# Performance work log

Measured on AMD Instinct MI355X. Metric: run time of the kernel, lower is better.

The kernel has to match this reference:

```python
import jax, jax.numpy as jnp
import numpy as np

N_ENT = 100000   # n_entities
N_REL = 40       # n_relations_ckg
D = 64           # embed_dim
L = 3            # n_layers
E = 1000000      # number of CKG triples (edges)


def setup_inputs() -> dict:
    key = jax.random.key(0)
    k = jax.random.split(key, 6)
    xavier = np.sqrt(6.0 / (D + D))  # xavier_uniform for square Linear
    return {
        "heads": jax.random.randint(k[0], (E,), 0, N_ENT),
        "rels": jax.random.randint(k[1], (E,), 0, N_REL),
        "tails": jax.random.randint(k[2], (E,), 0, N_ENT),
        "entity_embed": 0.01 * jax.random.normal(k[3], (N_ENT, D), dtype=jnp.float32),
        "rel_embeds": 0.01 * jax.random.normal(k[4], (L, N_REL, D), dtype=jnp.float32),
        "Ws": (jax.random.uniform(k[5], (L, D, D), minval=-1.0, maxval=1.0) * xavier).astype(jnp.float32),
    }


def _kgat_layer(h, heads, rels, tails, rel_emb, W):
    # h: [N, D]; heads/rels/tails: [E]; rel_emb: [n_rel, D]; W: [D, D] (nn.Linear weight)
    n = h.shape[0]
    e_h = h[heads]            # [E, D] gather
    e_t = h[tails]            # [E, D] gather
    e_r = rel_emb[rels]       # [E, D] gather
    # pi(h,r,t) = e_t . tanh(e_h + e_r)
    score = jnp.sum(e_t * jnp.tanh(e_h + e_r), axis=-1)          # [E]
    score = score - jax.lax.stop_gradient(jnp.max(score))        # global shift (detach)
    score_exp = jnp.exp(score)                                   # [E]
    score_sum = jax.ops.segment_sum(score_exp, heads, num_segments=n)  # [N]
    attn = score_exp / (score_sum[heads] + 1e-10)                # [E] per-head softmax
    agg = jax.ops.segment_sum(attn[:, None] * e_t, heads, num_segments=n)  # [N, D]
    out = (h + agg) @ W.T                                        # Linear, no bias
    return jax.nn.leaky_relu(out, negative_slope=0.2)            # dropout = identity (eval)


def reference(heads, rels, tails, entity_embed, rel_embeds, Ws):
    h = entity_embed
    all_layers = [h]
    for l in range(rel_embeds.shape[0]):
        h = _kgat_layer(h, heads, rels, tails, rel_embeds[l], Ws[l])
        all_layers.append(h)
    return jnp.concatenate(all_layers, axis=-1)  # [N, D*(L+1)]
```

## Files before the change

### kernel.cpp

```cpp
#include <hip/hip_runtime.h>

#define DD 64
#define ROW 256
#define CHUNK 1024

__global__ void k_copy_embed(const float* __restrict__ ent, float* __restrict__ out, int n_rows) {
    int idx = blockIdx.x * blockDim.x + threadIdx.x;
    int total = n_rows * 16;
    if (idx >= total) return;
    int n = idx >> 4, q = idx & 15;
    const float4* src = (const float4*)(ent + (long)n * DD);
    float4* dst = (float4*)(out + (long)n * ROW);
    dst[q] = src[q];
}

__global__ void k_count(const int* __restrict__ heads, int* __restrict__ counts, int nE) {
    int e = blockIdx.x * 256 + threadIdx.x;
    if (e >= nE) return;
    atomicAdd(counts + heads[e], 1);
}

__global__ __launch_bounds__(256) void k_scan_chunk(
        const int* __restrict__ counts, int* __restrict__ offs,
        int* __restrict__ partials, int n) {
    __shared__ int lds[256];
    int base = blockIdx.x * CHUNK;
    int t = threadIdx.x;
    int c[4]; int sum = 0;
    #pragma unroll
    for (int j = 0; j < 4; ++j) {
        int i = base + t * 4 + j;
        c[j] = (i < n) ? counts[i] : 0;
        sum += c[j];
    }
    lds[t] = sum; __syncthreads();
    for (int d = 1; d < 256; d <<= 1) {
        int v = (t >= d) ? lds[t - d] : 0;
        __syncthreads();
        lds[t] += v;
        __syncthreads();
    }
    int excl = lds[t] - sum;
    if (t == 255) partials[blockIdx.x] = lds[255];
    int run = excl;
    #pragma unroll
    for (int j = 0; j < 4; ++j) {
        int i = base + t * 4 + j;
        if (i < n) offs[i] = run;
        run += c[j];
    }
}

__global__ __launch_bounds__(128) void k_scan_part(int* __restrict__ partials, int nb) {
    __shared__ int lds[128];
    int t = threadIdx.x;
    int v = (t < nb) ? partials[t] : 0;
    lds[t] = v; __syncthreads();
    for (int d = 1; d < 128; d <<= 1) {
        int u = (t >= d) ? lds[t - d] : 0;
        __syncthreads();
        lds[t] += u;
        __syncthreads();
    }
    if (t < nb) partials[t] = lds[t] - v;
}

__global__ void k_scan_add(int* __restrict__ offs, int* __restrict__ running,
                           const int* __restrict__ partials, int n, int nE) {
    int i = blockIdx.x * 256 + threadIdx.x;
    if (i < n) {
        int v = offs[i] + partials[i >> 10];
        offs[i] = v;
        running[i] = v;
    } else if (i == n) {
        offs[n] = nE;
    }
}

__global__ void k_scatter(const int* __restrict__ heads, const int* __restrict__ rels,
                          const int* __restrict__ tails, int* __restrict__ running,
                          int* __restrict__ packed, int nE) {
    int e = blockIdx.x * 256 + threadIdx.x;
    if (e >= nE) return;
    int h = heads[e];
    int pos = atomicAdd(running + h, 1);
    packed[pos] = tails[e] | (rels[e] << 20);
}

__global__ __launch_bounds__(256) void k_layer(
        const int* __restrict__ offs, const int* __restrict__ packed,
        const float* __restrict__ hbase, const float* __restrict__ relemb,
        const float* __restrict__ W, float* __restrict__ outbase,
        int n_heads, int nE) {
    __shared__ float Wt[DD * 65];
    __shared__ float xs[4][DD];
    for (int idx = threadIdx.x; idx < DD * DD; idx += 256)
        Wt[(idx & 63) * 65 + (idx >> 6)] = W[idx];
    __syncthreads();

    int w = threadIdx.x >> 6, lane = threadIdx.x & 63;
    int g = lane >> 4, s = lane & 15;

    for (int hd = blockIdx.x * 4 + w; hd < n_heads; hd += gridDim.x * 4) {
        const float4 eh4 = *(const float4*)(hbase + (long)hd * ROW + 4 * s);
        float4 acc = make_float4(0.f, 0.f, 0.f, 0.f);
        float ssum = 0.f;
        int p0 = offs[hd], pe = offs[hd + 1];

        for (int cbase = p0; cbase < pe; cbase += 64) {
            int clen = min(pe - cbase, 64);
            int vAll = packed[min(cbase + lane, nE - 1)];

            int i0 = (g < clen) ? g : 0;
            int i1 = (4 + g < clen) ? 4 + g : 0;
            int v0 = __shfl(vAll, i0);
            int v1 = __shfl(vAll, i1);
            float4 tt0 = *(const float4*)(hbase + (long)(v0 & 0xFFFFF) * ROW + 4 * s);
            float4 rr0 = *(const float4*)(relemb + (v0 >> 20) * DD + 4 * s);
            float4 tt1 = *(const float4*)(hbase + (long)(v1 & 0xFFFFF) * ROW + 4 * s);
            float4 rr1 = *(const float4*)(relemb + (v1 >> 20) * DD + 4 * s);

            for (int i = 0; i < clen; i += 8) {
                int ia = i + 8 + g;  ia = (ia < clen) ? ia : 0;
                int ib = i + 12 + g; ib = (ib < clen) ? ib : 0;
                int va = __shfl(vAll, ia);
                int vb = __shfl(vAll, ib);
                float4 tta = *(const float4*)(hbase + (long)(va & 0xFFFFF) * ROW + 4 * s);
                float4 rra = *(const float4*)(relemb + (va >> 20) * DD + 4 * s);
                float4 ttb = *(const float4*)(hbase + (long)(vb & 0xFFFFF) * ROW + 4 * s);
                float4 rrb = *(const float4*)(relemb + (vb >> 20) * DD + 4 * s);

                {
                    float sc = 0.f;
                    #pragma unroll
                    for (int q = 0; q < 4; ++q) {
                        float xq = (&eh4.x)[q] + (&rr0.x)[q];
                        float t = __expf(2.f * xq);
                        float th = 1.f - 2.f * __builtin_amdgcn_rcpf(t + 1.f);
                        sc += (&tt0.x)[q] * th;
                    }
                    #pragma unroll
                    for (int off = 1; off <= 8; off <<= 1) sc += __shfl_xor(sc, off);
                    float se = ((i + g) < clen) ? __expf(sc) : 0.f;
                    ssum += se;
                    acc.x += se * tt0.x; acc.y += se * tt0.y;
                    acc.z += se * tt0.z; acc.w += se * tt0.w;
                }
                {
                    float sc = 0.f;
                    #pragma unroll
                    for (int q = 0; q < 4; ++q) {
                        float xq = (&eh4.x)[q] + (&rr1.x)[q];
                        float t = __expf(2.f * xq);
                        float th = 1.f - 2.f * __builtin_amdgcn_rcpf(t + 1.f);
                        sc += (&tt1.x)[q] * th;
                    }
                    #pragma unroll
                    for (int off = 1; off <= 8; off <<= 1) sc += __shfl_xor(sc, off);
                    float se = ((i + 4 + g) < clen) ? __expf(sc) : 0.f;
                    ssum += se;
                    acc.x += se * tt1.x; acc.y += se * tt1.y;
                    acc.z += se * tt1.z; acc.w += se * tt1.w;
                }
                tt0 = tta; rr0 = rra; tt1 = ttb; rr1 = rrb;
            }
        }

        #pragma unroll
        for (int off = 16; off <= 32; off <<= 1) {
            acc.x += __shfl_xor(acc.x, off);
            acc.y += __shfl_xor(acc.y, off);
            acc.z += __shfl_xor(acc.z, off);
            acc.w += __shfl_xor(acc.w, off);
            ssum  += __shfl_xor(ssum,  off);
        }
        float inv = 1.f / (ssum + 1e-10f);
        float4 x4;
        x4.x = eh4.x + acc.x * inv;  x4.y = eh4.y + acc.y * inv;
        x4.z = eh4.z + acc.z * inv;  x4.w = eh4.w + acc.w * inv;
        if (g == 0) *(float4*)(&xs[w][4 * s]) = x4;

        float y = 0.f;
        const float* xw = xs[w];
        #pragma unroll
        for (int k4 = 0; k4 < DD; k4 += 4) {
            float4 xv = *(const float4*)(xw + k4);
            y += xv.x * Wt[(k4 + 0) * 65 + lane];
            y += xv.y * Wt[(k4 + 1) * 65 + lane];
            y += xv.z * Wt[(k4 + 2) * 65 + lane];
            y += xv.w * Wt[(k4 + 3) * 65 + lane];
        }
        y = y >= 0.f ? y : 0.2f * y;
        outbase[(long)hd * ROW + lane] = y;
    }
}

extern "C" void kernel_launch(void* const* d_in, const int* in_sizes, int n_in,
                              void* d_out, int out_size, void* d_ws, size_t ws_size,
                              hipStream_t stream) {
    const int*   heads = (const int*)d_in[0];
    const int*   rels  = (const int*)d_in[1];
    const int*   tails = (const int*)d_in[2];
    const float* ent   = (const float*)d_in[3];
    const float* rel   = (const float*)d_in[4];
    const float* Ws    = (const float*)d_in[5];
    float* out = (float*)d_out;

    const int nE = in_sizes[0];
    const int N  = in_sizes[3] / DD;
    const int L  = in_sizes[5] / (DD * DD);
    const int NREL = in_sizes[4] / (L * DD);

    int* offs    = (int*)d_ws;
    int* running = offs + (N + 1);
    int* packed  = running + N;
    int* partials = packed + nE - 128;

    dim3 blk(256);
    int copy_blocks = (N * 16 + 255) / 256;
    int nchunks = (N + CHUNK - 1) / CHUNK;

    k_copy_embed<<<copy_blocks, blk, 0, stream>>>(ent, out, N);

    hipMemsetAsync(running, 0, (size_t)N * sizeof(int), stream);
    k_count<<<(nE + 255) / 256, blk, 0, stream>>>(heads, running, nE);
    k_scan_chunk<<<nchunks, blk, 0, stream>>>(running, offs, partials, N);
    k_scan_part<<<1, 128, 0, stream>>>(partials, nchunks);
    k_scan_add<<<(N + 1 + 255) / 256, blk, 0, stream>>>(offs, running, partials, N, nE);
    k_scatter<<<(nE + 255) / 256, blk, 0, stream>>>(heads, rels, tails, running, packed, nE);

    for (int l = 0; l < L; ++l) {
        k_layer<<<2048, blk, 0, stream>>>(
            offs, packed, out + l * DD, rel + (long)l * NREL * DD,
            Ws + (long)l * DD * DD, out + (l + 1) * DD, N, nE);
    }
}
```

Baseline: 503.4 us.

## Use polynomial tanh fast path, single-edge pipeline, and two-head batched matvec

Replaces the exp/rcp tanh with an odd minimax polynomial for small arguments, falling back to the exact form when any lane's argument exceeds a threshold. Given the small embedding values, the fallback should rarely fire. The edge loop now handles one edge group per iteration with a rolling prefetch depth of two. Each warp also processes two heads before a shared-memory matvec that reads W as float4 rows, which amortizes weight loads. The costs are an extra wave-wide vote per edge and shallower unrolling of the gather loop.

```diff
diff --git a/kernel.cpp b/kernel.cpp
--- a/kernel.cpp
+++ b/kernel.cpp
@@ -92,106 +92,111 @@
         const float* __restrict__ hbase, const float* __restrict__ relemb,
         const float* __restrict__ W, float* __restrict__ outbase,
         int n_heads, int nE) {
-    __shared__ float Wt[DD * 65];
-    __shared__ float xs[4][DD];
+    __shared__ float Wr[DD * 68];
+    __shared__ float xs[4][2][DD];
     for (int idx = threadIdx.x; idx < DD * DD; idx += 256)
-        Wt[(idx & 63) * 65 + (idx >> 6)] = W[idx];
+        Wr[(idx >> 6) * 68 + (idx & 63)] = W[idx];
     __syncthreads();
 
     int w = threadIdx.x >> 6, lane = threadIdx.x & 63;
     int g = lane >> 4, s = lane & 15;
-
-    for (int hd = blockIdx.x * 4 + w; hd < n_heads; hd += gridDim.x * 4) {
-        const float4 eh4 = *(const float4*)(hbase + (long)hd * ROW + 4 * s);
-        float4 acc = make_float4(0.f, 0.f, 0.f, 0.f);
-        float ssum = 0.f;
-        int p0 = offs[hd], pe = offs[hd + 1];
-
-        for (int cbase = p0; cbase < pe; cbase += 64) {
-            int clen = min(pe - cbase, 64);
-            int vAll = packed[min(cbase + lane, nE - 1)];
-
-            int i0 = (g < clen) ? g : 0;
-            int i1 = (4 + g < clen) ? 4 + g : 0;
-            int v0 = __shfl(vAll, i0);
-            int v1 = __shfl(vAll, i1);
-            float4 tt0 = *(const float4*)(hbase + (long)(v0 & 0xFFFFF) * ROW + 4 * s);
-            float4 rr0 = *(const float4*)(relemb + (v0 >> 20) * DD + 4 * s);
-            float4 tt1 = *(const float4*)(hbase + (long)(v1 & 0xFFFFF) * ROW + 4 * s);
-            float4 rr1 = *(const float4*)(relemb + (v1 >> 20) * DD + 4 * s);
-
-            for (int i = 0; i < clen; i += 8) {
-                int ia = i + 8 + g;  ia = (ia < clen) ? ia : 0;
-                int ib = i + 12 + g; ib = (ib < clen) ? ib : 0;
-                int va = __shfl(vAll, ia);
-                int vb = __shfl(vAll, ib);
-                float4 tta = *(const float4*)(hbase + (long)(va & 0xFFFFF) * ROW + 4 * s);
-                float4 rra = *(const float4*)(relemb + (va >> 20) * DD + 4 * s);
-                float4 ttb = *(const float4*)(hbase + (long)(vb & 0xFFFFF) * ROW + 4 * s);
-                float4 rrb = *(const float4*)(relemb + (vb >> 20) * DD + 4 * s);
-
-                {
-                    float sc = 0.f;
+    int wg = blockIdx.x * 4 + w;
+    int stride = gridDim.x * 4 * 2;
+
+    for (int hd0 = wg * 2; hd0 < n_heads; hd0 += stride) {
+        int nh = min(2, n_heads - hd0);
+
+        for (int hi = 0; hi < nh; ++hi) {
+            int hd = hd0 + hi;
+            const float4 eh4 = *(const float4*)(hbase + (long)hd * ROW + 4 * s);
+            float4 acc = make_float4(0.f, 0.f, 0.f, 0.f);
+            float ssum = 0.f;
+            int p0 = offs[hd], pe = offs[hd + 1];
+
+            for (int cbase = p0; cbase < pe; cbase += 64) {
+                int clen = min(pe - cbase, 64);
+                int vAll = packed[min(cbase + lane, nE - 1)];
+
+                int i0 = (g < clen) ? g : 0;
+                int i1 = (4 + g < clen) ? 4 + g : 0;
+                int v0 = __shfl(vAll, i0);
+                int v1 = __shfl(vAll, i1);
+                float4 tt0 = *(const float4*)(hbase + (long)(v0 & 0xFFFFF) * ROW + 4 * s);
+                float4 rr0 = *(const float4*)(relemb + (v0 >> 20) * DD + 4 * s);
+                float4 tt1 = *(const float4*)(hbase + (long)(v1 & 0xFFFFF) * ROW + 4 * s);
+                float4 rr1 = *(const float4*)(relemb + (v1 >> 20) * DD + 4 * s);
+
+                for (int i = 0; i < clen; i += 4) {
+                    int ipf = i + 8 + g; ipf = (ipf < clen) ? ipf : 0;
+                    int vp = __shfl(vAll, ipf);
+                    float4 ttp = *(const float4*)(hbase + (long)(vp & 0xFFFFF) * ROW + 4 * s);
+                    float4 rrp = *(const float4*)(relemb + (vp >> 20) * DD + 4 * s);
+
+                    float sc = 0.f, ax = 0.f;
                     #pragma unroll
                     for (int q = 0; q < 4; ++q) {
-                        float xq = (&eh4.x)[q] + (&rr0.x)[q];
-                        float t = __expf(2.f * xq);
-                        float th = 1.f - 2.f * __builtin_amdgcn_rcpf(t + 1.f);
-                        sc += (&tt0.x)[q] * th;
+                        float x = (&eh4.x)[q] + (&rr0.x)[q];
+                        float z = x * x;
+                        float p = fmaf(z, -5.70498872745e-3f, 2.06390887954e-2f);
+                        p = fmaf(z, p, -5.37397155531e-2f);
+                        p = fmaf(z, p, 1.33314422036e-1f);
+                        p = fmaf(z, p, -3.33332819422e-1f);
+                        float th = fmaf(x * z, p, x);
+                        ax = fmaxf(ax, fabsf(x));
+                        sc = fmaf((&tt0.x)[q], th, sc);
+                    }
+                    if (__any(ax > 0.625f)) {
+                        sc = 0.f;
+                        #pragma unroll
+                        for (int q = 0; q < 4; ++q) {
+                            float x = (&eh4.x)[q] + (&rr0.x)[q];
+                            float t = __expf(2.f * x);
+                            float th = 1.f - 2.f * __builtin_amdgcn_rcpf(t + 1.f);
+                            sc = fmaf((&tt0.x)[q], th, sc);
+                        }
                     }
                     #pragma unroll
                     for (int off = 1; off <= 8; off <<= 1) sc += __shfl_xor(sc, off);
                     float se = ((i + g) < clen) ? __expf(sc) : 0.f;
                     ssum += se;
-                    acc.x += se * tt0.x; acc.y += se * tt0.y;
-                    acc.z += se * tt0.z; acc.w += se * tt0.w;
+                    acc.x = fmaf(se, tt0.x, acc.x);
+                    acc.y = fmaf(se, tt0.y, acc.y);
+                    acc.z = fmaf(se, tt0.z, acc.z);
+                    acc.w = fmaf(se, tt0.w, acc.w);
+
+                    tt0 = tt1; rr0 = rr1; tt1 = ttp; rr1 = rrp;
                 }
-                {
-                    float sc = 0.f;
-                    #pragma unroll
-                    for (int q = 0; q < 4; ++q) {
-                        float xq = (&eh4.x)[q] + (&rr1.x)[q];
-                        float t = __expf(2.f * xq);
-                        float th = 1.f - 2.f * __builtin_amdgcn_rcpf(t + 1.f);
-                        sc += (&tt1.x)[q] * th;
-                    }
-                    #pragma unroll
-                    for (int off = 1; off <= 8; off <<= 1) sc += __shfl_xor(sc, off);
-                    float se = ((i + 4 + g) < clen) ? __expf(sc) : 0.f;
-                    ssum += se;
-                    acc.x += se * tt1.x; acc.y += se * tt1.y;
-                    acc.z += se * tt1.z; acc.w += se * tt1.w;
-                }
-                tt0 = tta; rr0 = rra; tt1 = ttb; rr1 = rrb;
             }
+
+            #pragma unroll
+            for (int off = 16; off <= 32; off <<= 1) {
+                acc.x += __shfl_xor(acc.x, off);
+                acc.y += __shfl_xor(acc.y, off);
+                acc.z += __shfl_xor(acc.z, off);
+                acc.w += __shfl_xor(acc.w, off);
+                ssum  += __shfl_xor(ssum,  off);
+            }
+            float inv = 1.f / (ssum + 1e-10f);
+            float4 x4;
+            x4.x = eh4.x + acc.x * inv;  x4.y = eh4.y + acc.y * inv;
+            x4.z = eh4.z + acc.z * inv;  x4.w = eh4.w + acc.w * inv;
+            if (g == 0) *(float4*)(&xs[w][hi][4 * s]) = x4;
         }
 
-        #pragma unroll
-        for (int off = 16; off <= 32; off <<= 1) {
-            acc.x += __shfl_xor(acc.x, off);
-            acc.y += __shfl_xor(acc.y, off);
-            acc.z += __shfl_xor(acc.z, off);
-            acc.w += __shfl_xor(acc.w, off);
-            ssum  += __shfl_xor(ssum,  off);
-        }
-        float inv = 1.f / (ssum + 1e-10f);
-        float4 x4;
-        x4.x = eh4.x + acc.x * inv;  x4.y = eh4.y + acc.y * inv;
-        x4.z = eh4.z + acc.z * inv;  x4.w = eh4.w + acc.w * inv;
-        if (g == 0) *(float4*)(&xs[w][4 * s]) = x4;
-
-        float y = 0.f;
-        const float* xw = xs[w];
+        float y0 = 0.f, y1 = 0.f;
+        const float* wrow = Wr + lane * 68;
         #pragma unroll
         for (int k4 = 0; k4 < DD; k4 += 4) {
-            float4 xv = *(const float4*)(xw + k4);
-            y += xv.x * Wt[(k4 + 0) * 65 + lane];
-            y += xv.y * Wt[(k4 + 1) * 65 + lane];
-            y += xv.z * Wt[(k4 + 2) * 65 + lane];
-            y += xv.w * Wt[(k4 + 3) * 65 + lane];
+            float4 wv = *(const float4*)(wrow + k4);
+            float4 a = *(const float4*)(&xs[w][0][k4]);
+            float4 b = *(const float4*)(&xs[w][1][k4]);
+            y0 += a.x * wv.x + a.y * wv.y + a.z * wv.z + a.w * wv.w;
+            y1 += b.x * wv.x + b.y * wv.y + b.z * wv.z + b.w * wv.w;
         }
-        y = y >= 0.f ? y : 0.2f * y;
-        outbase[(long)hd * ROW + lane] = y;
+        y0 = y0 >= 0.f ? y0 : 0.2f * y0;
+        y1 = y1 >= 0.f ? y1 : 0.2f * y1;
+        outbase[(long)hd0 * ROW + lane] = y0;
+        if (nh > 1) outbase[(long)(hd0 + 1) * ROW + lane] = y1;
     }
 }
 
```

Measured after the change: 607.7 us. 20.7% more time.
